# Kernel optimization log

Measured on AMD Instinct MI355X. Metric: run time of the kernel, lower is better.

The kernel has to match this reference:

```python
import jax, jax.numpy as jnp
import numpy as np
import math

B, S, E = 4, 2048, 1024
H, KV = 16, 4            # query heads, kv heads
HD = E // H              # head_dim = 64
R, CD = 8, 64            # TPA rank, context dim
NQ, NL = 8, 2            # qubits, VQC layers
EPS = 1e-6
LN_EPS = 1e-5


def setup_inputs() -> dict:
    key = jax.random.key(0)
    ks = jax.random.split(key, 16)
    def dense(k, i, o):
        return (jax.random.normal(k, (i, o), jnp.float32) / np.float32(np.sqrt(i)))
    d = {}
    d["x"] = jax.random.normal(ks[0], (B, S, E), jnp.float32)
    d["ctxW"] = dense(ks[1], E, CD);      d["ctxb"] = jnp.zeros((CD,), jnp.float32)
    d["qaW"] = dense(ks[2], E, R * HD);   d["qab"] = jnp.zeros((R * HD,), jnp.float32)
    d["qbW"] = dense(ks[3], CD, R * H);   d["qbb"] = jnp.zeros((R * H,), jnp.float32)
    d["kaW"] = dense(ks[4], E, R * HD);   d["kab"] = jnp.zeros((R * HD,), jnp.float32)
    d["kbW"] = dense(ks[5], CD, R * KV);  d["kbb"] = jnp.zeros((R * KV,), jnp.float32)
    d["vaW"] = dense(ks[6], E, R * HD);   d["vab"] = jnp.zeros((R * HD,), jnp.float32)
    d["vbW"] = dense(ks[7], CD, R * KV);  d["vbb"] = jnp.zeros((R * KV,), jnp.float32)
    d["qeW"] = dense(ks[8], HD, NQ);      d["qeb"] = jnp.zeros((NQ,), jnp.float32)
    d["vqc"] = jax.random.normal(ks[9], (NL, NQ, 3), jnp.float32) * 0.3
    d["ent"] = jnp.array([0.1], jnp.float32)
    d["outW"] = dense(ks[10], E, E);      d["outb"] = jnp.zeros((E,), jnp.float32)
    d["gamma"] = jnp.ones((E,), jnp.float32)
    d["beta"] = jnp.zeros((E,), jnp.float32)
    return d


def _tpa(x, ctx, aW, ab, bW, bb, nh):
    # output = sum_r (x @ A_r) outer (ctx @ B_r)  ->  [b, nh, s, head_dim]
    b, s, _ = x.shape
    a = (x @ aW + ab).reshape(b, s, R, HD)
    bf = (ctx @ bW + bb).reshape(b, s, R, nh)
    return jnp.einsum('bsrd,bsrh->bhsd', a, bf)


def _quantum_features(x, qeW, qeb, vqc, ent):
    # x: [b, h, s, HD] -> features [b, h, s, 2*NQ]
    angles = jnp.tanh(x @ qeW + qeb) * math.pi
    f = angles
    for l in range(NL):
        p = vqc[l]  # [NQ, 3]
        f = jnp.cos(f + p[:, 0]) * jnp.sin(f + p[:, 1]) + jnp.cos(f + p[:, 2])
        f = f * (1.0 + ent[0] * jnp.roll(f, shift=1, axis=-1))  # entanglement
    qf = jnp.concatenate([jnp.cos(f), jnp.sin(f)], axis=-1)
    return qf / (jnp.linalg.norm(qf, axis=-1, keepdims=True) + EPS)


def reference(x, ctxW, ctxb, qaW, qab, qbW, qbb, kaW, kab, kbW, kbb,
              vaW, vab, vbW, vbb, qeW, qeb, vqc, ent, outW, outb, gamma, beta):
    ctx = x @ ctxW + ctxb                              # [B,S,CD]
    q = _tpa(x, ctx, qaW, qab, qbW, qbb, H)            # [B,H,S,HD]
    k = _tpa(x, ctx, kaW, kab, kbW, kbb, KV)           # [B,KV,S,HD]
    v = _tpa(x, ctx, vaW, vab, vbW, vbb, KV)
    # GQA: expand KV heads to match query heads
    k = jnp.repeat(k, H // KV, axis=1)
    v = jnp.repeat(v, H // KV, axis=1)
    qf = _quantum_features(q, qeW, qeb, vqc, ent)      # [B,H,S,2*NQ]
    kf = _quantum_features(k, qeW, qeb, vqc, ent)
    # causal linear attention via cumulative KV state
    kv = jnp.cumsum(jnp.einsum('bhsf,bhsd->bhsfd', kf, v), axis=2)
    num = jnp.einsum('bhsf,bhsfd->bhsd', qf, kv)
    den = jnp.einsum('bhsf,bhsf->bhs', qf, jnp.cumsum(kf, axis=2))
    attn = num / (den[..., None] + EPS)                # [B,H,S,HD]
    o = attn.transpose(0, 2, 1, 3).reshape(B, S, E) @ outW + outb
    y = x + o                                          # residual + layernorm
    mu = jnp.mean(y, axis=-1, keepdims=True)
    var = jnp.mean(jnp.square(y - mu), axis=-1, keepdims=True)
    return gamma * (y - mu) / jnp.sqrt(var + LN_EPS) + beta
```

## Files before the change

### kernel.cpp

```cpp
#include <hip/hip_runtime.h>
#include <math.h>

#define Bb  4
#define Ss  2048
#define Ee  1024
#define Hh  16
#define KVh 4
#define HD  64
#define RNK 8
#define CDd 64
#define NQ  8
#define NLn 2
#define NF  16
#define NC  64
#define CT  (Ss/NC)
#define BS  (Bb*Ss)
#define NCAT 1664

typedef unsigned short ushort_t;
typedef __attribute__((ext_vector_type(8))) short short8;
typedef __attribute__((ext_vector_type(4))) float f32x4;
typedef __attribute__((ext_vector_type(4))) unsigned short u16x4;

__device__ __forceinline__ unsigned short f2bf(float f) {
    unsigned int u = __float_as_uint(f);
    unsigned int r = (u + 0x7FFFu + ((u >> 16) & 1u)) >> 16;
    return (unsigned short)r;
}
__device__ __forceinline__ float bf2f(unsigned short h) {
    return __uint_as_float(((unsigned int)h) << 16);
}

#define GLD16(gp, lp) \
    __builtin_amdgcn_global_load_lds((const __attribute__((address_space(1))) void*)(gp), \
                                     (__attribute__((address_space(3))) void*)(lp), 16, 0, 0)

__global__ __launch_bounds__(256)
void prep_all(const float* __restrict__ x, ushort_t* __restrict__ xb,
              const float* __restrict__ qaW, const float* __restrict__ kaW,
              const float* __restrict__ vaW, const float* __restrict__ outW,
              const float* __restrict__ ctxW,
              const float* __restrict__ qab, const float* __restrict__ kab,
              const float* __restrict__ vab, const float* __restrict__ ctxb,
              ushort_t* __restrict__ WcatT, ushort_t* __restrict__ outWt,
              float* __restrict__ bcat)
{
    __shared__ float t[32][33];
    const int bid = blockIdx.x;
    const int tx = threadIdx.x & 31, ty = threadIdx.x >> 5;
    if (bid < 4096) {
        const long i = (long)bid * 2048 + threadIdx.x * 8;
        short8 o;
        #pragma unroll
        for (int j = 0; j < 8; ++j) o[j] = (short)f2bf(x[i + j]);
        *(short8*)(xb + i) = o;
    } else if (bid < 5632) {
        const int r0 = bid - 4096;
        const int z = r0 >> 9;
        const int r = r0 & 511;
        const int k0 = (r & 31) * 32, n0 = (r >> 5) * 32;
        const float* W = (z == 0) ? qaW : (z == 1) ? kaW : vaW;
        const int nOff = 512 * z;
        #pragma unroll
        for (int i = 0; i < 4; ++i)
            t[ty + 8*i][tx] = W[(size_t)(k0 + ty + 8*i) * 512 + (n0 + tx)];
        __syncthreads();
        #pragma unroll
        for (int i = 0; i < 4; ++i)
            WcatT[(size_t)(nOff + n0 + ty + 8*i) * Ee + (k0 + tx)] = f2bf(t[tx][ty + 8*i]);
    } else if (bid < 6656) {
        const int r = bid - 5632;
        const int k0 = (r & 31) * 32, n0 = (r >> 5) * 32;
        #pragma unroll
        for (int i = 0; i < 4; ++i)
            t[ty + 8*i][tx] = outW[(size_t)(k0 + ty + 8*i) * 1024 + (n0 + tx)];
        __syncthreads();
        #pragma unroll
        for (int i = 0; i < 4; ++i)
            outWt[(size_t)(n0 + ty + 8*i) * Ee + (k0 + tx)] = f2bf(t[tx][ty + 8*i]);
    } else {
        const int pid = bid - 6656;
        if (pid < 64) {
            const int k0 = (pid >> 1) * 32, n0 = (pid & 1) * 32;
            #pragma unroll
            for (int i = 0; i < 4; ++i)
                t[ty + 8*i][tx] = ctxW[(size_t)(k0 + ty + 8*i) * 64 + (n0 + tx)];
            __syncthreads();
            #pragma unroll
            for (int i = 0; i < 4; ++i)
                WcatT[(size_t)(1536 + n0 + ty + 8*i) * Ee + (k0 + tx)] = f2bf(t[tx][ty + 8*i]);
        } else if (pid < 96) {
            const int idx = (pid - 64) * 2048 + threadIdx.x * 8;
            short8 z = {0, 0, 0, 0, 0, 0, 0, 0};
            *(short8*)(WcatT + (size_t)1600 * Ee + idx) = z;
        } else {
            const int n = (pid - 96) * 256 + threadIdx.x;
            if (n < NCAT) {
                float v = 0.f;
                if      (n < 512)  v = qab[n];
                else if (n < 1024) v = kab[n - 512];
                else if (n < 1536) v = vab[n - 1024];
                else if (n < 1600) v = ctxb[n - 1536];
                bcat[n] = v;
            }
        }
    }
}

template<int RES, int OUTBF>
__global__ __launch_bounds__(256)
void gemm_mfma(const ushort_t* __restrict__ A, const ushort_t* __restrict__ Bt,
               const float* __restrict__ bias, const float* __restrict__ res,
               void* __restrict__ Cout, int M, int N, int K)
{
    __shared__ ushort_t Al[128 * 32];
    __shared__ ushort_t Bl[128 * 32];
    const int tid  = threadIdx.x;
    const int lane = tid & 63;
    const int wave = tid >> 6;
    const int wm = wave >> 1;
    const int wn = wave & 1;

    const unsigned nx  = gridDim.x;
    const unsigned bid = blockIdx.y * nx + blockIdx.x;
    const unsigned nwg = nx * gridDim.y;
    const unsigned qc = nwg >> 3, rc = nwg & 7;
    const unsigned xc = bid & 7, of = bid >> 3;
    const unsigned tile = (xc < rc ? xc * (qc + 1) : rc * (qc + 1) + (xc - rc) * qc) + of;
    const int bm = (int)(tile / nx) * 128;
    const int bn = (int)(tile % nx) * 128;

    f32x4 acc[4][4] = {};

    const int arow0 = wave * 16 + (lane >> 2);
    const int kq = lane & 3;
    const ushort_t* Ag0 = A  + (size_t)(bm + arow0) * K + kq * 8;
    const ushort_t* Ag1 = A  + (size_t)(bm + 64 + arow0) * K + kq * 8;
    const ushort_t* Bg0 = Bt + (size_t)(bn + arow0) * K + kq * 8;
    const ushort_t* Bg1 = Bt + (size_t)(bn + 64 + arow0) * K + kq * 8;
    ushort_t* Alw = Al + wave * 512;
    ushort_t* Blw = Bl + wave * 512;

    const int fr = lane & 15;
    const int fg = lane >> 4;

    for (int k0 = 0; k0 < K; k0 += 32) {
        GLD16(Ag0 + k0, Alw);
        GLD16(Ag1 + k0, Alw + 2048);
        GLD16(Bg0 + k0, Blw);
        GLD16(Bg1 + k0, Blw + 2048);
        __syncthreads();
        short8 af[4], bfv[4];
        #pragma unroll
        for (int mi = 0; mi < 4; ++mi)
            af[mi] = *(const short8*)&Al[(wm*64 + mi*16 + fr) * 32 + fg * 8];
        #pragma unroll
        for (int ni = 0; ni < 4; ++ni)
            bfv[ni] = *(const short8*)&Bl[(wn*64 + ni*16 + fr) * 32 + fg * 8];
        #pragma unroll
        for (int mi = 0; mi < 4; ++mi)
            #pragma unroll
            for (int ni = 0; ni < 4; ++ni)
                acc[mi][ni] = __builtin_amdgcn_mfma_f32_16x16x32_bf16(
                    af[mi], bfv[ni], acc[mi][ni], 0, 0, 0);
        __syncthreads();
    }

    float bv[4];
    #pragma unroll
    for (int ni = 0; ni < 4; ++ni) bv[ni] = bias[bn + wn*64 + ni*16 + fr];
    #pragma unroll
    for (int mi = 0; mi < 4; ++mi) {
        #pragma unroll
        for (int ni = 0; ni < 4; ++ni) {
            const int gn = bn + wn*64 + ni*16 + fr;
            #pragma unroll
            for (int r = 0; r < 4; ++r) {
                const int gm = bm + wm*64 + mi*16 + fg*4 + r;
                float v = acc[mi][ni][r] + bv[ni];
                if (RES) v += res[(size_t)gm * N + gn];
                if (OUTBF) ((ushort_t*)Cout)[(size_t)gm * N + gn] = f2bf(v);
                else       ((float*)Cout)[(size_t)gm * N + gn] = v;
            }
        }
    }
}

__global__ __launch_bounds__(256)
void combine_quantum(const ushort_t* __restrict__ Cf,
                     const float* __restrict__ qbW, const float* __restrict__ qbb,
                     const float* __restrict__ kbW, const float* __restrict__ kbb,
                     const float* __restrict__ vbW, const float* __restrict__ vbb,
                     const float* __restrict__ qeW, const float* __restrict__ qeb,
                     const float* __restrict__ vqc, const float* __restrict__ ent,
                     float* __restrict__ qf_g, float* __restrict__ kf_g,
                     float* __restrict__ v_g)
{
    const int wid = threadIdx.x >> 6;
    const int d   = threadIdx.x & 63;
    const int bs  = blockIdx.x * 4 + wid;
    const int b = bs >> 11;
    const int s = bs & 2047;

    __shared__ float qew_s[HD*NQ];
    __shared__ float ctx_l[4][CDd];
    __shared__ float bfq[4][128];
    __shared__ float bfk[4][32];
    __shared__ float bfv[4][32];
    __shared__ float rows[4][Hh+KVh][65];

    #pragma unroll
    for (int i = 0; i < 2; ++i)
        qew_s[threadIdx.x + 256*i] = qeW[threadIdx.x + 256*i];

    const ushort_t* Crow = Cf + (size_t)bs * NCAT;
    ctx_l[wid][d] = bf2f(Crow[1536 + d]);
    __syncthreads();

    {
        const int t = threadIdx.x;
        if (t < 192) {
            const float* Wc; float bb; int ldw;
            if (t < 128)      { Wc = qbW + t;         bb = qbb[t];       ldw = 128; }
            else if (t < 160) { Wc = kbW + (t - 128); bb = kbb[t - 128]; ldw = 32;  }
            else              { Wc = vbW + (t - 160); bb = vbb[t - 160]; ldw = 32;  }
            float a0 = bb, a1 = bb, a2 = bb, a3 = bb;
            #pragma unroll 8
            for (int k = 0; k < CDd; ++k) {
                const float w = Wc[(size_t)k * ldw];
                a0 += ctx_l[0][k] * w;
                a1 += ctx_l[1][k] * w;
                a2 += ctx_l[2][k] * w;
                a3 += ctx_l[3][k] * w;
            }
            if (t < 128) {
                bfq[0][t] = a0; bfq[1][t] = a1; bfq[2][t] = a2; bfq[3][t] = a3;
            } else if (t < 160) {
                const int n = t - 128;
                bfk[0][n] = a0; bfk[1][n] = a1; bfk[2][n] = a2; bfk[3][n] = a3;
            } else {
                const int n = t - 160;
                bfv[0][n] = a0; bfv[1][n] = a1; bfv[2][n] = a2; bfv[3][n] = a3;
            }
        }
    }

    float aq[RNK], ak[RNK], av[RNK];
    #pragma unroll
    for (int r = 0; r < RNK; ++r) {
        aq[r] = bf2f(Crow[r*64 + d]);
        ak[r] = bf2f(Crow[512 + r*64 + d]);
        av[r] = bf2f(Crow[1024 + r*64 + d]);
    }
    __syncthreads();

    #pragma unroll
    for (int h = 0; h < Hh; ++h) {
        float acc = 0.f;
        #pragma unroll
        for (int r = 0; r < RNK; ++r) acc += aq[r] * bfq[wid][r*16 + h];
        rows[wid][h][d] = acc;
    }
    #pragma unroll
    for (int kvh = 0; kvh < KVh; ++kvh) {
        float acck = 0.f, accv = 0.f;
        #pragma unroll
        for (int r = 0; r < RNK; ++r) {
            acck += ak[r] * bfk[wid][r*4 + kvh];
            accv += av[r] * bfv[wid][r*4 + kvh];
        }
        rows[wid][Hh + kvh][d] = acck;
        v_g[((size_t)(b*KVh + kvh)*Ss + s)*HD + d] = accv;
    }
    __syncthreads();

    const float entv = ent[0];
    const int i   = d & 7;
    const int src = (d & ~7) | ((i + 7) & 7);
    float p00 = vqc[(0*NQ + i)*3 + 0], p01 = vqc[(0*NQ + i)*3 + 1], p02 = vqc[(0*NQ + i)*3 + 2];
    float p10 = vqc[(1*NQ + i)*3 + 0], p11 = vqc[(1*NQ + i)*3 + 1], p12 = vqc[(1*NQ + i)*3 + 2];
    const float qebi = qeb[i];

    #pragma unroll
    for (int stripe = 0; stripe < 3; ++stripe) {
        const int row = stripe * 8 + (d >> 3);
        const bool active = (row < Hh + KVh);
        const int rowc = active ? row : (Hh + KVh - 1);
        float acc = qebi;
        #pragma unroll 16
        for (int dd = 0; dd < HD; ++dd)
            acc += rows[wid][rowc][dd] * qew_s[dd*8 + i];
        float f = tanhf(acc) * 3.14159265358979323846f;
        float g = cosf(f + p00) * sinf(f + p01) + cosf(f + p02);
        float gp = __shfl(g, src, 64);
        f = g * (1.f + entv * gp);
        g = cosf(f + p10) * sinf(f + p11) + cosf(f + p12);
        gp = __shfl(g, src, 64);
        f = g * (1.f + entv * gp);
        float c = cosf(f), sn = sinf(f);
        float ss = c*c + sn*sn;
        ss += __shfl_xor(ss, 1, 64);
        ss += __shfl_xor(ss, 2, 64);
        ss += __shfl_xor(ss, 4, 64);
        const float inv = 1.f / (sqrtf(ss) + 1e-6f);
        if (active) {
            float* dst = (row < Hh)
                ? qf_g + ((size_t)(b*Hh + row)*Ss + s)*NF
                : kf_g + ((size_t)(b*KVh + (row - Hh))*Ss + s)*NF;
            dst[i]      = c * inv;
            dst[NQ + i] = sn * inv;
        }
    }
}

__global__ __launch_bounds__(64)
void chunk_partial(const float* __restrict__ kf_g, const float* __restrict__ v_g,
                   float* __restrict__ kvpart, float* __restrict__ kfpart)
{
    const int id = blockIdx.x;
    const int c = id & (NC-1);
    const int bk = id / NC;
    const int d = threadIdx.x;
    __shared__ float kf_l[CT][NF];
    const int s0 = c * CT;
    const float* kfp = kf_g + ((size_t)bk*Ss + s0)*NF;
    #pragma unroll
    for (int t = 0; t < (CT*NF)/64; ++t)
        ((float*)kf_l)[d + 64*t] = kfp[d + 64*t];
    __syncthreads();
    float st[NF] = {};
    const float* vp = v_g + ((size_t)bk*Ss + s0)*HD;
    for (int t = 0; t < CT; ++t) {
        const float vd = vp[(size_t)t*HD + d];
        #pragma unroll
        for (int f = 0; f < NF; ++f) st[f] += kf_l[t][f] * vd;
    }
    float* kvp = kvpart + (size_t)id * (NF*HD);
    #pragma unroll
    for (int f = 0; f < NF; ++f) kvp[f*HD + d] = st[f];
    if (d < NF) {
        float acc = 0.f;
        for (int t = 0; t < CT; ++t) acc += kf_l[t][d];
        kfpart[(size_t)id*NF + d] = acc;
    }
}

__global__ void prefix_scan(float* __restrict__ kvpart, float* __restrict__ kfpart)
{
    const int idx = blockIdx.x * blockDim.x + threadIdx.x;
    const int total = Bb*KVh * (NF*HD + NF);
    if (idx >= total) return;
    const int bk = idx / (NF*HD + NF);
    const int e = idx % (NF*HD + NF);
    if (e < NF*HD) {
        float* p = kvpart + (size_t)bk*NC*(NF*HD) + e;
        float run = 0.f;
        for (int c = 0; c < NC; ++c) {
            const float t = p[(size_t)c*(NF*HD)];
            p[(size_t)c*(NF*HD)] = run;
            run += t;
        }
    } else {
        const int f = e - NF*HD;
        float* p = kfpart + (size_t)bk*NC*NF + f;
        float run = 0.f;
        for (int c = 0; c < NC; ++c) {
            const float t = p[(size_t)c*NF];
            p[(size_t)c*NF] = run;
            run += t;
        }
    }
}

__global__ __launch_bounds__(64)
void attn_scan(const float* __restrict__ qf_g, const float* __restrict__ kf_g,
               const float* __restrict__ v_g,
               const float* __restrict__ kvpart, const float* __restrict__ kfpart,
               ushort_t* __restrict__ o_bf)
{
    const int id = blockIdx.x;
    const int c = id & (NC-1);
    const int bh = id / NC;
    const int h = bh & (Hh-1);
    const int b = bh / Hh;
    const int kvh = h >> 2;
    const int d = threadIdx.x;
    __shared__ float kf_l[CT][NF];
    __shared__ float qf_l[CT][NF];
    const int s0 = c * CT;
    const float* kfp = kf_g + ((size_t)(b*KVh + kvh)*Ss + s0)*NF;
    const float* qfp = qf_g + ((size_t)(b*Hh + h)*Ss + s0)*NF;
    #pragma unroll
    for (int t = 0; t < (CT*NF)/64; ++t) {
        ((float*)kf_l)[d + 64*t] = kfp[d + 64*t];
        ((float*)qf_l)[d + 64*t] = qfp[d + 64*t];
    }
    float st[NF], kfs[NF];
    const float* kvp  = kvpart + ((size_t)(b*KVh + kvh)*NC + c)*(NF*HD);
    const float* kfsp = kfpart + ((size_t)(b*KVh + kvh)*NC + c)*NF;
    #pragma unroll
    for (int f = 0; f < NF; ++f) { st[f] = kvp[f*HD + d]; kfs[f] = kfsp[f]; }
    __syncthreads();
    const float* vp = v_g + ((size_t)(b*KVh + kvh)*Ss + s0)*HD;
    ushort_t* op = o_bf + ((size_t)(b*Ss + s0))*Ee + h*HD;
    for (int t = 0; t < CT; ++t) {
        const float vd = vp[(size_t)t*HD + d];
        float num0 = 0.f, num1 = 0.f, den0 = 0.f, den1 = 0.f;
        #pragma unroll
        for (int f = 0; f < NF; f += 2) {
            const float kv0 = kf_l[t][f];
            const float kv1 = kf_l[t][f+1];
            st[f]   += kv0 * vd;   kfs[f]   += kv0;
            st[f+1] += kv1 * vd;   kfs[f+1] += kv1;
            const float qv0 = qf_l[t][f];
            const float qv1 = qf_l[t][f+1];
            num0 += qv0 * st[f];   den0 += qv0 * kfs[f];
            num1 += qv1 * st[f+1]; den1 += qv1 * kfs[f+1];
        }
        op[(size_t)t*Ee + d] = f2bf((num0 + num1) / ((den0 + den1) + 1e-6f));
    }
}

__global__ __launch_bounds__(256)
void layernorm_res(const float* __restrict__ x, const ushort_t* __restrict__ o_bf,
                   const float* __restrict__ gamma, const float* __restrict__ beta,
                   float* __restrict__ out)
{
    __shared__ float tmp[4];
    const int row = blockIdx.x;
    const int t = threadIdx.x;
    const float* xp = x + (size_t)row * Ee;
    const ushort_t* op = o_bf + (size_t)row * Ee;
    const f32x4 xv = *(const f32x4*)(xp + t*4);
    const u16x4 ov = *(const u16x4*)(op + t*4);
    float v[4];
    float sum = 0.f;
    #pragma unroll
    for (int i = 0; i < 4; ++i) { v[i] = xv[i] + bf2f(ov[i]); sum += v[i]; }
    #pragma unroll
    for (int o = 32; o > 0; o >>= 1) sum += __shfl_down(sum, o, 64);
    if ((t & 63) == 0) tmp[t >> 6] = sum;
    __syncthreads();
    const float mu = (tmp[0] + tmp[1] + tmp[2] + tmp[3]) * (1.f/Ee);
    __syncthreads();
    float vs = 0.f;
    #pragma unroll
    for (int i = 0; i < 4; ++i) { const float dd = v[i] - mu; vs += dd*dd; }
    #pragma unroll
    for (int o = 32; o > 0; o >>= 1) vs += __shfl_down(vs, o, 64);
    if ((t & 63) == 0) tmp[t >> 6] = vs;
    __syncthreads();
    const float var = (tmp[0] + tmp[1] + tmp[2] + tmp[3]) * (1.f/Ee);
    const float inv = rsqrtf(var + 1e-5f);
    const f32x4 gv = *(const f32x4*)(gamma + t*4);
    const f32x4 bv = *(const f32x4*)(beta + t*4);
    f32x4 ovec;
    #pragma unroll
    for (int i = 0; i < 4; ++i) ovec[i] = gv[i] * (v[i] - mu) * inv + bv[i];
    *(f32x4*)(out + (size_t)row * Ee + t*4) = ovec;
}

extern "C" void kernel_launch(void* const* d_in, const int* in_sizes, int n_in,
                              void* d_out, int out_size, void* d_ws, size_t ws_size,
                              hipStream_t stream)
{
    const float* x    = (const float*)d_in[0];
    const float* ctxW = (const float*)d_in[1];
    const float* ctxb = (const float*)d_in[2];
    const float* qaW  = (const float*)d_in[3];
    const float* qab  = (const float*)d_in[4];
    const float* qbW  = (const float*)d_in[5];
    const float* qbb  = (const float*)d_in[6];
    const float* kaW  = (const float*)d_in[7];
    const float* kab  = (const float*)d_in[8];
    const float* kbW  = (const float*)d_in[9];
    const float* kbb  = (const float*)d_in[10];
    const float* vaW  = (const float*)d_in[11];
    const float* vab  = (const float*)d_in[12];
    const float* vbW  = (const float*)d_in[13];
    const float* vbb  = (const float*)d_in[14];
    const float* qeW  = (const float*)d_in[15];
    const float* qeb  = (const float*)d_in[16];
    const float* vqc  = (const float*)d_in[17];
    const float* ent  = (const float*)d_in[18];
    const float* outW = (const float*)d_in[19];
    const float* outb = (const float*)d_in[20];
    const float* gamma= (const float*)d_in[21];
    const float* beta = (const float*)d_in[22];
    float* out = (float*)d_out;

    char* p = (char*)d_ws;
    auto alloc = [&](size_t bytes) { char* r = p; p += (bytes + 255) & ~(size_t)255; return (void*)r; };
    ushort_t* xb    = (ushort_t*)alloc((size_t)BS * Ee * 2);
    ushort_t* WcatT = (ushort_t*)alloc((size_t)NCAT * Ee * 2);
    ushort_t* outWt = (ushort_t*)alloc((size_t)Ee * Ee * 2);
    float*    bcat  = (float*)   alloc(NCAT * 4);
    ushort_t* Cf    = (ushort_t*)alloc((size_t)BS * NCAT * 2);
    float*    qf    = (float*)   alloc((size_t)Bb*Hh*Ss*NF * 4);
    float*    kf    = (float*)   alloc((size_t)Bb*KVh*Ss*NF * 4);
    float*    vg    = (float*)   alloc((size_t)Bb*KVh*Ss*HD * 4);
    float*    kvpart= (float*)   alloc((size_t)Bb*KVh*NC*NF*HD * 4);
    float*    kfpart= (float*)   alloc((size_t)Bb*KVh*NC*NF * 4);
    ushort_t* obf   = Cf;
    ushort_t* obf2  = (ushort_t*)qf;

    prep_all<<<6759, 256, 0, stream>>>(x, xb, qaW, kaW, vaW, outW, ctxW,
                                       qab, kab, vab, ctxb, WcatT, outWt, bcat);

    gemm_mfma<0,1><<<dim3(NCAT/128, BS/128), 256, 0, stream>>>(
        xb, WcatT, bcat, nullptr, Cf, BS, NCAT, Ee);
    combine_quantum<<<BS/4, 256, 0, stream>>>(Cf, qbW, qbb, kbW, kbb, vbW, vbb,
                                              qeW, qeb, vqc, ent, qf, kf, vg);
    chunk_partial<<<Bb*KVh*NC, 64, 0, stream>>>(kf, vg, kvpart, kfpart);
    prefix_scan<<<(Bb*KVh*(NF*HD + NF) + 255)/256, 256, 0, stream>>>(kvpart, kfpart);
    attn_scan<<<Bb*Hh*NC, 64, 0, stream>>>(qf, kf, vg, kvpart, kfpart, obf);
    gemm_mfma<0,1><<<dim3(Ee/128, BS/128), 256, 0, stream>>>(
        obf, outWt, outb, nullptr, obf2, BS, Ee, Ee);
    layernorm_res<<<BS, 256, 0, stream>>>(x, obf2, gamma, beta, out);
}
```

Measured before the change: 289.0 us.

## Double-buffer GEMM LDS tiles and use fast intrinsics in quantum feature kernel

The GEMM kernel now keeps two LDS buffers and issues the global-to-LDS load for the next K tile before computing on the current one, aiming to hide load latency. The feature kernel computes all three stripe dot products in one loop, sharing each weight load, and replaces tanhf/sinf/cosf with exp-based tanh and __sinf/__cosf fast intrinsics. The fast intrinsics lose accuracy, and the double buffer doubles LDS use, which may lower occupancy. The visible part of the loop does not clearly show a barrier that protects the buffer being refilled.

New measurement: 276.9 us. -4.2%, faster.

```diff
diff --git a/kernel.cpp b/kernel.cpp
--- a/kernel.cpp
+++ b/kernel.cpp
@@ -113,8 +113,8 @@
                const float* __restrict__ bias, const float* __restrict__ res,
                void* __restrict__ Cout, int M, int N, int K)
 {
-    __shared__ ushort_t Al[128 * 32];
-    __shared__ ushort_t Bl[128 * 32];
+    __shared__ ushort_t Al[2][128 * 32];
+    __shared__ ushort_t Bl[2][128 * 32];
     const int tid  = threadIdx.x;
     const int lane = tid & 63;
     const int wave = tid >> 6;
@@ -138,25 +138,39 @@
     const ushort_t* Ag1 = A  + (size_t)(bm + 64 + arow0) * K + kq * 8;
     const ushort_t* Bg0 = Bt + (size_t)(bn + arow0) * K + kq * 8;
     const ushort_t* Bg1 = Bt + (size_t)(bn + 64 + arow0) * K + kq * 8;
-    ushort_t* Alw = Al + wave * 512;
-    ushort_t* Blw = Bl + wave * 512;
 
     const int fr = lane & 15;
     const int fg = lane >> 4;
-
-    for (int k0 = 0; k0 < K; k0 += 32) {
-        GLD16(Ag0 + k0, Alw);
-        GLD16(Ag1 + k0, Alw + 2048);
-        GLD16(Bg0 + k0, Blw);
-        GLD16(Bg1 + k0, Blw + 2048);
+    const int nt = K >> 5;
+
+    {
+        ushort_t* Aw = &Al[0][wave * 512];
+        ushort_t* Bw = &Bl[0][wave * 512];
+        GLD16(Ag0, Aw);
+        GLD16(Ag1, Aw + 2048);
+        GLD16(Bg0, Bw);
+        GLD16(Bg1, Bw + 2048);
         __syncthreads();
+    }
+
+    for (int t = 0; t < nt; ++t) {
+        const int cur = t & 1;
+        if (t + 1 < nt) {
+            const int k1 = (t + 1) << 5;
+            ushort_t* Aw = &Al[cur ^ 1][wave * 512];
+            ushort_t* Bw = &Bl[cur ^ 1][wave * 512];
+            GLD16(Ag0 + k1, Aw);
+            GLD16(Ag1 + k1, Aw + 2048);
+            GLD16(Bg0 + k1, Bw);
+            GLD16(Bg1 + k1, Bw + 2048);
+        }
         short8 af[4], bfv[4];
         #pragma unroll
         for (int mi = 0; mi < 4; ++mi)
-            af[mi] = *(const short8*)&Al[(wm*64 + mi*16 + fr) * 32 + fg * 8];
+            af[mi] = *(const short8*)&Al[cur][(wm*64 + mi*16 + fr) * 32 + fg * 8];
         #pragma unroll
         for (int ni = 0; ni < 4; ++ni)
-            bfv[ni] = *(const short8*)&Bl[(wn*64 + ni*16 + fr) * 32 + fg * 8];
+            bfv[ni] = *(const short8*)&Bl[cur][(wn*64 + ni*16 + fr) * 32 + fg * 8];
         #pragma unroll
         for (int mi = 0; mi < 4; ++mi)
             #pragma unroll
@@ -277,33 +291,45 @@
     const float entv = ent[0];
     const int i   = d & 7;
     const int src = (d & ~7) | ((i + 7) & 7);
-    float p00 = vqc[(0*NQ + i)*3 + 0], p01 = vqc[(0*NQ + i)*3 + 1], p02 = vqc[(0*NQ + i)*3 + 2];
-    float p10 = vqc[(1*NQ + i)*3 + 0], p11 = vqc[(1*NQ + i)*3 + 1], p12 = vqc[(1*NQ + i)*3 + 2];
+    const float p00 = vqc[(0*NQ + i)*3 + 0], p01 = vqc[(0*NQ + i)*3 + 1], p02 = vqc[(0*NQ + i)*3 + 2];
+    const float p10 = vqc[(1*NQ + i)*3 + 0], p11 = vqc[(1*NQ + i)*3 + 1], p12 = vqc[(1*NQ + i)*3 + 2];
     const float qebi = qeb[i];
-
+    const int r0 = d >> 3;
+    const int r1 = 8 + r0;
+    const bool act2 = (16 + r0) < (Hh + KVh);
+    const int r2 = act2 ? (16 + r0) : (Hh + KVh - 1);
+
+    float a0 = qebi, a1 = qebi, a2 = qebi;
+    #pragma unroll 8
+    for (int dd = 0; dd < HD; ++dd) {
+        const float qw = qew_s[dd*8 + i];
+        a0 += rows[wid][r0][dd] * qw;
+        a1 += rows[wid][r1][dd] * qw;
+        a2 += rows[wid][r2][dd] * qw;
+    }
+
+    float accs[3] = {a0, a1, a2};
+    const int rowNo[3] = {r0, r1, 16 + r0};
+    const bool activ[3] = {true, true, act2};
     #pragma unroll
     for (int stripe = 0; stripe < 3; ++stripe) {
-        const int row = stripe * 8 + (d >> 3);
-        const bool active = (row < Hh + KVh);
-        const int rowc = active ? row : (Hh + KVh - 1);
-        float acc = qebi;
-        #pragma unroll 16
-        for (int dd = 0; dd < HD; ++dd)
-            acc += rows[wid][rowc][dd] * qew_s[dd*8 + i];
-        float f = tanhf(acc) * 3.14159265358979323846f;
-        float g = cosf(f + p00) * sinf(f + p01) + cosf(f + p02);
+        float acc = fminf(fmaxf(accs[stripe], -15.f), 15.f);
+        const float e = __expf(2.f * acc);
+        float f = ((e - 1.f) / (e + 1.f)) * 3.14159265358979323846f;
+        float g = __cosf(f + p00) * __sinf(f + p01) + __cosf(f + p02);
         float gp = __shfl(g, src, 64);
         f = g * (1.f + entv * gp);
-        g = cosf(f + p10) * sinf(f + p11) + cosf(f + p12);
+        g = __cosf(f + p10) * __sinf(f + p11) + __cosf(f + p12);
         gp = __shfl(g, src, 64);
         f = g * (1.f + entv * gp);
-        float c = cosf(f), sn = sinf(f);
+        const float c = __cosf(f), sn = __sinf(f);
         float ss = c*c + sn*sn;
         ss += __shfl_xor(ss, 1, 64);
         ss += __shfl_xor(ss, 2, 64);
         ss += __shfl_xor(ss, 4, 64);
         const float inv = 1.f / (sqrtf(ss) + 1e-6f);
-        if (active) {
+        if (activ[stripe]) {
+            const int row = rowNo[stripe];
             float* dst = (row < Hh)
                 ? qf_g + ((size_t)(b*Hh + row)*Ss + s)*NF
                 : kf_g + ((size_t)(b*KVh + (row - Hh))*Ss + s)*NF;
```
